# Kernel optimization log

Hardware: AMD Instinct MI355X
Metric: run time of the kernel (lower is better)

The kernel has to match this reference:

```python
import jax, jax.numpy as jnp
import numpy as np

B, L, D, H = 32, 512, 512, 8


def setup_inputs() -> dict:
    key = jax.random.key(0)
    ks = jax.random.split(key, 6)
    s = 0.02
    return {
        "queries": jax.random.normal(ks[0], (B, L, D), jnp.float32),
        "keys": jax.random.normal(ks[1], (B, L, D), jnp.float32),
        "Wq": jax.random.normal(ks[2], (D, D), jnp.float32) * s,
        "bq": jnp.zeros((D,), jnp.float32),
        "Wk": jax.random.normal(ks[3], (D, D), jnp.float32) * s,
        "bk": jnp.zeros((D,), jnp.float32),
        "Wv": jax.random.normal(ks[4], (D, D), jnp.float32) * s,
        "bv": jnp.zeros((D,), jnp.float32),
        "causality": 1,
    }


def reference(queries, keys, Wq, bq, Wk, bk, Wv, bv, causality):
    b, lq, d = queries.shape
    lk = keys.shape[1]
    dh = d // H

    # torch Linear: x @ W.T + b
    Q = queries @ Wq.T + bq
    K = keys @ Wk.T + bk
    V = keys @ Wv.T + bv

    # chunk along feature dim then cat along batch == head-major [H, B, L, dh]
    def split_heads(x, l):
        return x.reshape(b, l, H, dh).transpose(2, 0, 1, 3)

    Qh = split_heads(Q, lq)
    Kh = split_heads(K, lk)
    Vh = split_heads(V, lk)

    scores = jnp.einsum('hbqd,hbkd->hbqk', Qh, Kh) / jnp.sqrt(jnp.asarray(dh, queries.dtype))

    # sign-based key padding mask: zero rows of `keys` get -inf scores
    key_mask = jnp.sign(jnp.sum(jnp.abs(keys), axis=-1))  # [B, Lk]
    scores = jnp.where(key_mask[None, :, None, :] == 0, -jnp.inf, scores)

    if causality:
        tril = jnp.tril(jnp.ones((lq, lk), dtype=bool))
        scores = jnp.where(tril[None, None, :, :], scores, -jnp.inf)

    w = jax.nn.softmax(scores, axis=-1)
    w = jnp.nan_to_num(w, nan=0.0, posinf=0.0, neginf=0.0)

    # sign-based query mask multiplied AFTER softmax
    query_mask = jnp.sign(jnp.sum(jnp.abs(queries), axis=-1))  # [B, Lq]
    w = w * query_mask[None, :, :, None]

    attention_weights = w.transpose(1, 0, 2, 3)  # [B, H, Lq, Lk]

    # dropout is identity in eval mode
    out = jnp.einsum('hbqk,hbkd->hbqd', w, Vh)          # [H, B, Lq, dh]
    out = out.transpose(1, 2, 0, 3).reshape(b, lq, d)    # head-major concat on feature dim
    return out, attention_weights
```

## Files before the change

kernel.cpp:

```cpp
#include <hip/hip_runtime.h>
#include <math.h>

typedef short short8 __attribute__((ext_vector_type(8)));
typedef short short4v __attribute__((ext_vector_type(4)));
typedef float float4v __attribute__((ext_vector_type(4)));

__device__ __forceinline__ short f2bf(float f) {
    union { float f; unsigned u; } v; v.f = f;
    unsigned r = (v.u + 0x7FFFu + ((v.u >> 16) & 1u)) >> 16;
    return (short)r;
}

__device__ __forceinline__ void async16(const short* g, short* l) {
    __builtin_amdgcn_global_load_lds(
        (const __attribute__((address_space(1))) unsigned*)g,
        (__attribute__((address_space(3))) unsigned*)l, 16, 0, 0);
}

__global__ void cvt_kernel(const float* __restrict__ src, short* __restrict__ dst, int n4) {
    int i = blockIdx.x * blockDim.x + threadIdx.x;
    if (i < n4) {
        float4v v = ((const float4v*)src)[i];
        short4v o;
        o[0] = f2bf(v[0]); o[1] = f2bf(v[1]); o[2] = f2bf(v[2]); o[3] = f2bf(v[3]);
        ((short4v*)dst)[i] = o;
    }
}

__global__ __launch_bounds__(256) void cvtmask_kernel(
    const float* __restrict__ q, const float* __restrict__ k,
    short* __restrict__ qb, short* __restrict__ kb,
    float* __restrict__ qm, float* __restrict__ km) {
    int tid = threadIdx.x;
    int lane = tid & 63, wv = tid >> 6;
    int row = blockIdx.x * 4 + wv;
    const float* src; short* dst; float* msk; int r;
    if (row < 16384) { src = q; dst = qb; msk = qm; r = row; }
    else             { src = k; dst = kb; msk = km; r = row - 16384; }
    const float4v* p = (const float4v*)(src + (size_t)r * 512);
    float4v a = p[lane];
    float4v b = p[lane + 64];
    short4v o1, o2;
    o1[0] = f2bf(a[0]); o1[1] = f2bf(a[1]); o1[2] = f2bf(a[2]); o1[3] = f2bf(a[3]);
    o2[0] = f2bf(b[0]); o2[1] = f2bf(b[1]); o2[2] = f2bf(b[2]); o2[3] = f2bf(b[3]);
    short4v* d4 = (short4v*)(dst + (size_t)r * 512);
    d4[lane] = o1;
    d4[lane + 64] = o2;
    float s = fabsf(a[0]) + fabsf(a[1]) + fabsf(a[2]) + fabsf(a[3])
            + fabsf(b[0]) + fabsf(b[1]) + fabsf(b[2]) + fabsf(b[3]);
    #pragma unroll
    for (int off = 1; off < 64; off <<= 1) s += __shfl_xor(s, off, 64);
    if (lane == 0) msk[r] = (s > 0.f) ? 1.f : 0.f;
}

__global__ __launch_bounds__(256) void proj_kernel(
    const short* __restrict__ Xq, const short* __restrict__ Xk,
    const short* __restrict__ Wqp, const short* __restrict__ Wkp, const short* __restrict__ Wvp,
    const float* __restrict__ bqp, const float* __restrict__ bkp, const float* __restrict__ bvp,
    short* __restrict__ Qo, short* __restrict__ Ko, short* __restrict__ Vo) {
    __shared__ short As[128 * 32];
    __shared__ short Bs[128 * 32];
    int z = blockIdx.z;
    const short* X    = (z == 0) ? Xq  : Xk;
    const short* W    = (z == 0) ? Wqp : (z == 1) ? Wkp : Wvp;
    const float* bias = (z == 0) ? bqp : (z == 1) ? bkp : bvp;
    short* out        = (z == 0) ? Qo  : (z == 1) ? Ko  : Vo;

    int tid = threadIdx.x;
    int lane = tid & 63, wv = tid >> 6;
    int col = lane & 15, quad = lane >> 4;
    int m0 = blockIdx.x * 128;
    int n0 = blockIdx.y * 128;
    int msub = (wv & 1) * 64, nsub = (wv >> 1) * 64;

    float4v acc[4][4];
    #pragma unroll
    for (int mt = 0; mt < 4; ++mt)
        #pragma unroll
        for (int nt = 0; nt < 4; ++nt) { acc[mt][nt][0]=0.f; acc[mt][nt][1]=0.f; acc[mt][nt][2]=0.f; acc[mt][nt][3]=0.f; }

    int rowS = tid >> 2;
    int seg  = tid & 3;
    const short* gA0 = X + (size_t)(m0 + rowS) * 512 + seg * 8;
    const short* gA1 = X + (size_t)(m0 + 64 + rowS) * 512 + seg * 8;
    const short* gB0 = W + (size_t)(n0 + rowS) * 512 + seg * 8;
    const short* gB1 = W + (size_t)(n0 + 64 + rowS) * 512 + seg * 8;
    short* lA0 = As + (size_t)tid * 8;
    short* lA1 = As + (size_t)(256 + tid) * 8;
    short* lB0 = Bs + (size_t)tid * 8;
    short* lB1 = Bs + (size_t)(256 + tid) * 8;

    for (int k0 = 0; k0 < 512; k0 += 32) {
        __syncthreads();
        async16(gA0 + k0, lA0);
        async16(gA1 + k0, lA1);
        async16(gB0 + k0, lB0);
        async16(gB1 + k0, lB1);
        __syncthreads();
        short8 a[4], b[4];
        #pragma unroll
        for (int mt = 0; mt < 4; ++mt)
            a[mt] = *(const short8*)(As + (msub + mt * 16 + col) * 32 + quad * 8);
        #pragma unroll
        for (int nt = 0; nt < 4; ++nt)
            b[nt] = *(const short8*)(Bs + (nsub + nt * 16 + col) * 32 + quad * 8);
        #pragma unroll
        for (int mt = 0; mt < 4; ++mt)
            #pragma unroll
            for (int nt = 0; nt < 4; ++nt)
                acc[mt][nt] = __builtin_amdgcn_mfma_f32_16x16x32_bf16(a[mt], b[nt], acc[mt][nt], 0, 0, 0);
    }

    #pragma unroll
    for (int nt = 0; nt < 4; ++nt) {
        float bv = bias[n0 + nsub + nt * 16 + col];
        #pragma unroll
        for (int mt = 0; mt < 4; ++mt) {
            #pragma unroll
            for (int r = 0; r < 4; ++r) {
                int m = m0 + msub + mt * 16 + quad * 4 + r;
                out[(size_t)m * 512 + n0 + nsub + nt * 16 + col] = f2bf(acc[mt][nt][r] + bv);
            }
        }
    }
}

__global__ __launch_bounds__(256) void attn_kernel(
    const short* __restrict__ Q, const short* __restrict__ K, const short* __restrict__ V,
    const float* __restrict__ qmask, const float* __restrict__ kmask,
    const int* __restrict__ caus, float* __restrict__ out, float* __restrict__ aw) {
    __shared__ short vt[64 * 72];
    __shared__ short wl[4 * 16 * 72];

    int tid = threadIdx.x;
    int lane = tid & 63, wv = tid >> 6;
    int col = lane & 15, quad = lane >> 4;
    int qt = blockIdx.x, h = blockIdx.y, b = blockIdx.z;
    int q0 = qt * 64 + wv * 16;
    size_t rowbase = (size_t)b * 512;
    bool causal = (*caus) != 0;

    short8 aQ0, aQ1;
    {
        const short* qp = Q + (rowbase + q0 + col) * 512 + h * 64 + quad * 8;
        aQ0 = *(const short8*)(qp);
        aQ1 = *(const short8*)(qp + 32);
    }

    float4v sc[32];
    const short* kp = K + (rowbase + col) * 512 + h * 64 + quad * 8;
    const float* kmp = kmask + b * 512;
    #pragma unroll
    for (int t = 0; t < 32; ++t) {
        short8 b0 = *(const short8*)(kp + (size_t)(t * 16) * 512);
        short8 b1 = *(const short8*)(kp + (size_t)(t * 16) * 512 + 32);
        float4v s; s[0]=0.f; s[1]=0.f; s[2]=0.f; s[3]=0.f;
        s = __builtin_amdgcn_mfma_f32_16x16x32_bf16(aQ0, b0, s, 0, 0, 0);
        s = __builtin_amdgcn_mfma_f32_16x16x32_bf16(aQ1, b1, s, 0, 0, 0);
        int kcol = t * 16 + col;
        float km = kmp[kcol];
        #pragma unroll
        for (int r = 0; r < 4; ++r) {
            float v = s[r] * 0.125f;
            int qg = q0 + quad * 4 + r;
            bool masked = (km == 0.f) || (causal && (kcol > qg));
            sc[t][r] = masked ? -INFINITY : v;
        }
    }

    float mx[4], sm[4], inv[4];
    #pragma unroll
    for (int r = 0; r < 4; ++r) mx[r] = -INFINITY;
    #pragma unroll
    for (int t = 0; t < 32; ++t)
        #pragma unroll
        for (int r = 0; r < 4; ++r) mx[r] = fmaxf(mx[r], sc[t][r]);
    #pragma unroll
    for (int r = 0; r < 4; ++r) {
        #pragma unroll
        for (int off = 1; off < 16; off <<= 1) mx[r] = fmaxf(mx[r], __shfl_xor(mx[r], off, 64));
    }
    #pragma unroll
    for (int r = 0; r < 4; ++r) sm[r] = 0.f;
    #pragma unroll
    for (int t = 0; t < 32; ++t)
        #pragma unroll
        for (int r = 0; r < 4; ++r) {
            float s = sc[t][r];
            float e = (s == -INFINITY) ? 0.f : __expf(s - mx[r]);
            sc[t][r] = e;
            sm[r] += e;
        }
    #pragma unroll
    for (int r = 0; r < 4; ++r) {
        #pragma unroll
        for (int off = 1; off < 16; off <<= 1) sm[r] += __shfl_xor(sm[r], off, 64);
    }
    const float* qmp = qmask + b * 512;
    #pragma unroll
    for (int r = 0; r < 4; ++r) {
        float qm = qmp[q0 + quad * 4 + r];
        inv[r] = (sm[r] > 0.f) ? (qm / sm[r]) : 0.f;
    }
    #pragma unroll
    for (int t = 0; t < 32; ++t)
        #pragma unroll
        for (int r = 0; r < 4; ++r) sc[t][r] *= inv[r];

    float* awp = aw + ((size_t)b * 8 + h) * 512 * 512;
    #pragma unroll
    for (int t = 0; t < 32; ++t) {
        int kcol = t * 16 + col;
        #pragma unroll
        for (int r = 0; r < 4; ++r) {
            int qg = q0 + quad * 4 + r;
            awp[(size_t)qg * 512 + kcol] = sc[t][r];
        }
    }

    float4v O[4];
    #pragma unroll
    for (int nt = 0; nt < 4; ++nt) { O[nt][0]=0.f; O[nt][1]=0.f; O[nt][2]=0.f; O[nt][3]=0.f; }
    short* wlw = wl + wv * (16 * 72);
    #pragma unroll
    for (int c = 0; c < 8; ++c) {
        __syncthreads();
        #pragma unroll
        for (int i = 0; i < 16; ++i) {
            int idx = i * 256 + tid;
            int kk = idx >> 6, d = idx & 63;
            vt[d * 72 + kk] = V[(rowbase + c * 64 + kk) * 512 + h * 64 + d];
        }
        #pragma unroll
        for (int tl = 0; tl < 4; ++tl) {
            #pragma unroll
            for (int r = 0; r < 4; ++r)
                wlw[(quad * 4 + r) * 72 + tl * 16 + col] = f2bf(sc[c * 4 + tl][r]);
        }
        __syncthreads();
        #pragma unroll
        for (int sub = 0; sub < 2; ++sub) {
            short8 aW = *(const short8*)(wlw + col * 72 + sub * 32 + quad * 8);
            #pragma unroll
            for (int nt = 0; nt < 4; ++nt) {
                short8 bV = *(const short8*)(vt + (nt * 16 + col) * 72 + sub * 32 + quad * 8);
                O[nt] = __builtin_amdgcn_mfma_f32_16x16x32_bf16(aW, bV, O[nt], 0, 0, 0);
            }
        }
    }
    #pragma unroll
    for (int nt = 0; nt < 4; ++nt) {
        #pragma unroll
        for (int r = 0; r < 4; ++r) {
            int qg = q0 + quad * 4 + r;
            out[(rowbase + qg) * 512 + h * 64 + nt * 16 + col] = O[nt][r];
        }
    }
}

extern "C" void kernel_launch(void* const* d_in, const int* in_sizes, int n_in,
                              void* d_out, int out_size, void* d_ws, size_t ws_size,
                              hipStream_t stream) {
    const float* queries = (const float*)d_in[0];
    const float* keys    = (const float*)d_in[1];
    const float* Wq      = (const float*)d_in[2];
    const float* bq      = (const float*)d_in[3];
    const float* Wk      = (const float*)d_in[4];
    const float* bk      = (const float*)d_in[5];
    const float* Wv      = (const float*)d_in[6];
    const float* bv      = (const float*)d_in[7];
    const int*   caus    = (const int*)d_in[8];

    const size_t NE = (size_t)16384 * 512;
    short* qbf = (short*)d_ws;
    short* kbf = qbf + NE;
    short* Qb  = kbf + NE;
    short* Kb  = Qb + NE;
    short* Vb  = Kb + NE;
    short* wqb = Vb + NE;
    short* wkb = wqb + 512 * 512;
    short* wvb = wkb + 512 * 512;
    float* qm  = (float*)(wvb + 512 * 512);
    float* km  = qm + 32 * 512;

    cvtmask_kernel<<<8192, 256, 0, stream>>>(queries, keys, qbf, kbf, qm, km);
    cvt_kernel<<<256, 256, 0, stream>>>(Wq, wqb, 65536);
    cvt_kernel<<<256, 256, 0, stream>>>(Wk, wkb, 65536);
    cvt_kernel<<<256, 256, 0, stream>>>(Wv, wvb, 65536);
    dim3 pg(128, 4, 3);
    proj_kernel<<<pg, 256, 0, stream>>>(qbf, kbf, wqb, wkb, wvb, bq, bk, bv, Qb, Kb, Vb);
    float* outp = (float*)d_out;
    float* awp  = outp + 8388608;
    dim3 ag(8, 8, 32);
    attn_kernel<<<ag, 256, 0, stream>>>(Qb, Kb, Vb, qm, km, caus, outp, awp);
}
```

Baseline: 540.2 us.

## Transpose score MFMA for vectorized weight stores; widen projection K-tile and vector V loads

The score MFMA is swapped so K supplies the A operand and Q the B operand. Each lane then owns one query row and four consecutive keys, which lets the attention-weight output be written as float4 vectors and cuts the row-reduction shuffles to two steps. The V tile is loaded with 16-byte vector reads, and the weight fragments go to LDS as short4 stores. The projection GEMM K-tile doubles to 64 to halve barrier count, and the attention grid is reordered to put batch*head first. Costs are more LDS in the projection and possible bank conflicts on the transposed V scatter.

```diff
diff --git a/kernel.cpp b/kernel.cpp
--- a/kernel.cpp
+++ b/kernel.cpp
@@ -58,8 +58,8 @@
     const short* __restrict__ Wqp, const short* __restrict__ Wkp, const short* __restrict__ Wvp,
     const float* __restrict__ bqp, const float* __restrict__ bkp, const float* __restrict__ bvp,
     short* __restrict__ Qo, short* __restrict__ Ko, short* __restrict__ Vo) {
-    __shared__ short As[128 * 32];
-    __shared__ short Bs[128 * 32];
+    __shared__ short As[128 * 64];
+    __shared__ short Bs[128 * 64];
     int z = blockIdx.z;
     const short* X    = (z == 0) ? Xq  : Xk;
     const short* W    = (z == 0) ? Wqp : (z == 1) ? Wkp : Wvp;
@@ -79,36 +79,36 @@
         #pragma unroll
         for (int nt = 0; nt < 4; ++nt) { acc[mt][nt][0]=0.f; acc[mt][nt][1]=0.f; acc[mt][nt][2]=0.f; acc[mt][nt][3]=0.f; }
 
-    int rowS = tid >> 2;
-    int seg  = tid & 3;
-    const short* gA0 = X + (size_t)(m0 + rowS) * 512 + seg * 8;
-    const short* gA1 = X + (size_t)(m0 + 64 + rowS) * 512 + seg * 8;
-    const short* gB0 = W + (size_t)(n0 + rowS) * 512 + seg * 8;
-    const short* gB1 = W + (size_t)(n0 + 64 + rowS) * 512 + seg * 8;
-    short* lA0 = As + (size_t)tid * 8;
-    short* lA1 = As + (size_t)(256 + tid) * 8;
-    short* lB0 = Bs + (size_t)tid * 8;
-    short* lB1 = Bs + (size_t)(256 + tid) * 8;
-
-    for (int k0 = 0; k0 < 512; k0 += 32) {
-        __syncthreads();
-        async16(gA0 + k0, lA0);
-        async16(gA1 + k0, lA1);
-        async16(gB0 + k0, lB0);
-        async16(gB1 + k0, lB1);
-        __syncthreads();
-        short8 a[4], b[4];
-        #pragma unroll
-        for (int mt = 0; mt < 4; ++mt)
-            a[mt] = *(const short8*)(As + (msub + mt * 16 + col) * 32 + quad * 8);
-        #pragma unroll
-        for (int nt = 0; nt < 4; ++nt)
-            b[nt] = *(const short8*)(Bs + (nsub + nt * 16 + col) * 32 + quad * 8);
-        #pragma unroll
-        for (int mt = 0; mt < 4; ++mt)
+    int rowS = tid >> 3;
+    int seg  = tid & 7;
+    const short* gA = X + (size_t)(m0 + rowS) * 512 + seg * 8;
+    const short* gB = W + (size_t)(n0 + rowS) * 512 + seg * 8;
+    short* lA = As + (size_t)tid * 8;
+    short* lB = Bs + (size_t)tid * 8;
+
+    for (int k0 = 0; k0 < 512; k0 += 64) {
+        __syncthreads();
+        #pragma unroll
+        for (int j = 0; j < 4; ++j) {
+            async16(gA + (size_t)(j * 32) * 512 + k0, lA + j * 2048);
+            async16(gB + (size_t)(j * 32) * 512 + k0, lB + j * 2048);
+        }
+        __syncthreads();
+        #pragma unroll
+        for (int ksub = 0; ksub < 2; ++ksub) {
+            short8 a[4], b[4];
+            #pragma unroll
+            for (int mt = 0; mt < 4; ++mt)
+                a[mt] = *(const short8*)(As + (msub + mt * 16 + col) * 64 + ksub * 32 + quad * 8);
             #pragma unroll
             for (int nt = 0; nt < 4; ++nt)
-                acc[mt][nt] = __builtin_amdgcn_mfma_f32_16x16x32_bf16(a[mt], b[nt], acc[mt][nt], 0, 0, 0);
+                b[nt] = *(const short8*)(Bs + (nsub + nt * 16 + col) * 64 + ksub * 32 + quad * 8);
+            #pragma unroll
+            for (int mt = 0; mt < 4; ++mt)
+                #pragma unroll
+                for (int nt = 0; nt < 4; ++nt)
+                    acc[mt][nt] = __builtin_amdgcn_mfma_f32_16x16x32_bf16(a[mt], b[nt], acc[mt][nt], 0, 0, 0);
+        }
     }
 
     #pragma unroll
@@ -135,87 +135,71 @@
     int tid = threadIdx.x;
     int lane = tid & 63, wv = tid >> 6;
     int col = lane & 15, quad = lane >> 4;
-    int qt = blockIdx.x, h = blockIdx.y, b = blockIdx.z;
+    int bh = blockIdx.x, qt = blockIdx.y;
+    int b = bh >> 3, h = bh & 7;
     int q0 = qt * 64 + wv * 16;
     size_t rowbase = (size_t)b * 512;
     bool causal = (*caus) != 0;
 
-    short8 aQ0, aQ1;
+    short8 bQ0, bQ1;
     {
         const short* qp = Q + (rowbase + q0 + col) * 512 + h * 64 + quad * 8;
-        aQ0 = *(const short8*)(qp);
-        aQ1 = *(const short8*)(qp + 32);
+        bQ0 = *(const short8*)(qp);
+        bQ1 = *(const short8*)(qp + 32);
     }
 
     float4v sc[32];
     const short* kp = K + (rowbase + col) * 512 + h * 64 + quad * 8;
     const float* kmp = kmask + b * 512;
+    int qg = q0 + col;
     #pragma unroll
     for (int t = 0; t < 32; ++t) {
-        short8 b0 = *(const short8*)(kp + (size_t)(t * 16) * 512);
-        short8 b1 = *(const short8*)(kp + (size_t)(t * 16) * 512 + 32);
+        short8 aK0 = *(const short8*)(kp + (size_t)(t * 16) * 512);
+        short8 aK1 = *(const short8*)(kp + (size_t)(t * 16) * 512 + 32);
         float4v s; s[0]=0.f; s[1]=0.f; s[2]=0.f; s[3]=0.f;
-        s = __builtin_amdgcn_mfma_f32_16x16x32_bf16(aQ0, b0, s, 0, 0, 0);
-        s = __builtin_amdgcn_mfma_f32_16x16x32_bf16(aQ1, b1, s, 0, 0, 0);
-        int kcol = t * 16 + col;
-        float km = kmp[kcol];
+        s = __builtin_amdgcn_mfma_f32_16x16x32_bf16(aK0, bQ0, s, 0, 0, 0);
+        s = __builtin_amdgcn_mfma_f32_16x16x32_bf16(aK1, bQ1, s, 0, 0, 0);
+        int kb = t * 16 + quad * 4;
+        float4v km4 = *(const float4v*)(kmp + kb);
         #pragma unroll
         for (int r = 0; r < 4; ++r) {
             float v = s[r] * 0.125f;
-            int qg = q0 + quad * 4 + r;
-            bool masked = (km == 0.f) || (causal && (kcol > qg));
+            bool masked = (km4[r] == 0.f) || (causal && (kb + r > qg));
             sc[t][r] = masked ? -INFINITY : v;
         }
     }
 
-    float mx[4], sm[4], inv[4];
-    #pragma unroll
-    for (int r = 0; r < 4; ++r) mx[r] = -INFINITY;
+    float mx = -INFINITY;
     #pragma unroll
     for (int t = 0; t < 32; ++t)
         #pragma unroll
-        for (int r = 0; r < 4; ++r) mx[r] = fmaxf(mx[r], sc[t][r]);
-    #pragma unroll
-    for (int r = 0; r < 4; ++r) {
-        #pragma unroll
-        for (int off = 1; off < 16; off <<= 1) mx[r] = fmaxf(mx[r], __shfl_xor(mx[r], off, 64));
-    }
-    #pragma unroll
-    for (int r = 0; r < 4; ++r) sm[r] = 0.f;
+        for (int r = 0; r < 4; ++r) mx = fmaxf(mx, sc[t][r]);
+    mx = fmaxf(mx, __shfl_xor(mx, 16, 64));
+    mx = fmaxf(mx, __shfl_xor(mx, 32, 64));
+    float sm = 0.f;
     #pragma unroll
     for (int t = 0; t < 32; ++t)
         #pragma unroll
         for (int r = 0; r < 4; ++r) {
             float s = sc[t][r];
-            float e = (s == -INFINITY) ? 0.f : __expf(s - mx[r]);
+            float e = (s == -INFINITY) ? 0.f : __expf(s - mx);
             sc[t][r] = e;
-            sm[r] += e;
-        }
-    #pragma unroll
-    for (int r = 0; r < 4; ++r) {
-        #pragma unroll
-        for (int off = 1; off < 16; off <<= 1) sm[r] += __shfl_xor(sm[r], off, 64);
-    }
-    const float* qmp = qmask + b * 512;
-    #pragma unroll
-    for (int r = 0; r < 4; ++r) {
-        float qm = qmp[q0 + quad * 4 + r];
-        inv[r] = (sm[r] > 0.f) ? (qm / sm[r]) : 0.f;
-    }
+            sm += e;
+        }
+    sm += __shfl_xor(sm, 16, 64);
+    sm += __shfl_xor(sm, 32, 64);
+    float qmv = qmask[b * 512 + qg];
+    float inv = (sm > 0.f) ? (qmv / sm) : 0.f;
     #pragma unroll
     for (int t = 0; t < 32; ++t)
         #pragma unroll
-        for (int r = 0; r < 4; ++r) sc[t][r] *= inv[r];
-
-    float* awp = aw + ((size_t)b * 8 + h) * 512 * 512;
-    #pragma unroll
-    for (int t = 0; t < 32; ++t) {
-        int kcol = t * 16 + col;
-        #pragma unroll
-        for (int r = 0; r < 4; ++r) {
-            int qg = q0 + quad * 4 + r;
-            awp[(size_t)qg * 512 + kcol] = sc[t][r];
-        }
+        for (int r = 0; r < 4; ++r) sc[t][r] *= inv;
+
+    {
+        float* awr = aw + ((size_t)b * 8 + h) * 512 * 512 + (size_t)qg * 512 + quad * 4;
+        #pragma unroll
+        for (int t = 0; t < 32; ++t)
+            *(float4v*)(awr + t * 16) = sc[t];
     }
 
     float4v O[4];
@@ -226,16 +210,21 @@
     for (int c = 0; c < 8; ++c) {
         __syncthreads();
         #pragma unroll
-        for (int i = 0; i < 16; ++i) {
+        for (int i = 0; i < 2; ++i) {
             int idx = i * 256 + tid;
-            int kk = idx >> 6, d = idx & 63;
-            vt[d * 72 + kk] = V[(rowbase + c * 64 + kk) * 512 + h * 64 + d];
+            int kk = idx >> 3, sg = idx & 7;
+            short8 v8 = *(const short8*)(V + (rowbase + c * 64 + kk) * 512 + h * 64 + sg * 8);
+            #pragma unroll
+            for (int j = 0; j < 8; ++j)
+                vt[(sg * 8 + j) * 72 + kk] = v8[j];
         }
         #pragma unroll
         for (int tl = 0; tl < 4; ++tl) {
-            #pragma unroll
-            for (int r = 0; r < 4; ++r)
-                wlw[(quad * 4 + r) * 72 + tl * 16 + col] = f2bf(sc[c * 4 + tl][r]);
+            int t = c * 4 + tl;
+            short4v w4;
+            #pragma unroll
+            for (int r = 0; r < 4; ++r) w4[r] = f2bf(sc[t][r]);
+            *(short4v*)(wlw + col * 72 + tl * 16 + quad * 4) = w4;
         }
         __syncthreads();
         #pragma unroll
@@ -252,8 +241,8 @@
     for (int nt = 0; nt < 4; ++nt) {
         #pragma unroll
         for (int r = 0; r < 4; ++r) {
-            int qg = q0 + quad * 4 + r;
-            out[(rowbase + qg) * 512 + h * 64 + nt * 16 + col] = O[nt][r];
+            int qq = q0 + quad * 4 + r;
+            out[(rowbase + qq) * 512 + h * 64 + nt * 16 + col] = O[nt][r];
         }
     }
 }
@@ -291,6 +280,6 @@
     proj_kernel<<<pg, 256, 0, stream>>>(qbf, kbf, wqb, wkb, wvb, bq, bk, bv, Qb, Kb, Vb);
     float* outp = (float*)d_out;
     float* awp  = outp + 8388608;
-    dim3 ag(8, 8, 32);
+    dim3 ag(256, 8);
     attn_kernel<<<ag, 256, 0, stream>>>(Qb, Kb, Vb, qm, km, caus, outp, awp);
 }
```

Result: faster. 513.5 us (-4.9%).
